# Kernel optimization log

Hardware: AMD Instinct MI355X
Metric: run time of the kernel (lower is better)

Reference implementation:

```python
import jax, jax.numpy as jnp
import numpy as np

N_TOKENS, MODEL_DIM, NUM_EXPERTS = 65536, 1024, 64
CAPACITY_FACTOR = 1.0


def setup_inputs() -> dict:
    key = jax.random.key(0)
    k1, k2 = jax.random.split(key)
    x = jax.random.normal(k1, (N_TOKENS, MODEL_DIM), dtype=jnp.float32)
    # gate projection weight, torch Linear stores [out_features, in_features]
    wg = jax.random.normal(k2, (NUM_EXPERTS, MODEL_DIM), dtype=jnp.float32) * (1.0 / np.sqrt(MODEL_DIM))
    return {"x": x, "wg": wg}


def reference(x, wg):
    N, E = x.shape[0], wg.shape[0]
    logits = x @ wg.T                              # [N, E]
    # training-branch capacity: capacity_factor * ceil(N / E)
    capacity = int(CAPACITY_FACTOR * ((N + E - 1) // E))
    indices1_s = jnp.argmax(logits, axis=1)        # [N] top-1 expert per token
    gates = jax.nn.softmax(logits, axis=1)         # [N, E]
    mask1 = jax.nn.one_hot(indices1_s, E, dtype=gates.dtype)  # [N, E]
    gates1_s = jnp.sum(gates * mask1, axis=1)      # [N] gate value of chosen expert
    # locations1_s[i] = number of earlier tokens routed to the same expert
    # (exclusive prefix count = inclusive cumsum - 1 at the selected column)
    locations1 = jnp.cumsum(mask1, axis=0) - 1.0   # [N, E]
    locations1_s = jnp.sum(locations1 * mask1, axis=1).astype(jnp.int32)
    # auxiliary load-balance loss (float32 branch of the original)
    me = jnp.sum(gates, axis=0)                    # [E]
    ce = jnp.sum(mask1, axis=0)                    # [E]
    l_aux = jnp.sum(me * ce) * (E / (N * N))
    return (l_aux, indices1_s.astype(jnp.int32), capacity, locations1_s, gates1_s, E)
```

## Files before the change

### kernel.cpp

```cpp
#include <hip/hip_runtime.h>

#define NT 65536
#define MD 1024
#define NE 64
#define BK 32

__global__ __launch_bounds__(256) void gate_kernel(
    const float* __restrict__ x, const float* __restrict__ wg,
    float* __restrict__ out, int* __restrict__ idx_ws,
    float* __restrict__ me, float* __restrict__ ce)
{
    __shared__ __align__(16) float smem[2 * BK * 68];
    float (*as)[68] = (float (*)[68])smem;
    float (*bs)[68] = (float (*)[68])(smem + BK * 68);

    const int tid = threadIdx.x;
    const int tx = tid & 15;
    const int ty = tid >> 4;
    const int t0 = blockIdx.x * 64;

    float acc[4][4];
#pragma unroll
    for (int i = 0; i < 4; ++i)
#pragma unroll
        for (int j = 0; j < 4; ++j) acc[i][j] = 0.f;

    for (int k0 = 0; k0 < MD; k0 += BK) {
#pragma unroll
        for (int l = 0; l < 2; ++l) {
            int flat = tid + l * 256;
            int r = flat >> 3;
            int q = flat & 7;
            float4 v = *(const float4*)(x + (size_t)(t0 + r) * MD + k0 + q * 4);
            as[q * 4 + 0][r] = v.x; as[q * 4 + 1][r] = v.y;
            as[q * 4 + 2][r] = v.z; as[q * 4 + 3][r] = v.w;
            float4 w = *(const float4*)(wg + (size_t)r * MD + k0 + q * 4);
            bs[q * 4 + 0][r] = w.x; bs[q * 4 + 1][r] = w.y;
            bs[q * 4 + 2][r] = w.z; bs[q * 4 + 3][r] = w.w;
        }
        __syncthreads();
#pragma unroll
        for (int k = 0; k < BK; ++k) {
            float4 a = *(const float4*)&as[k][ty * 4];
            float4 b = *(const float4*)&bs[k][tx * 4];
            float av[4] = {a.x, a.y, a.z, a.w};
            float bv[4] = {b.x, b.y, b.z, b.w};
#pragma unroll
            for (int i = 0; i < 4; ++i)
#pragma unroll
                for (int j = 0; j < 4; ++j) acc[i][j] += av[i] * bv[j];
        }
        __syncthreads();
    }

    float* lt  = smem;
    float* inv = smem + 4160;
    int*   hist = (int*)(smem + 4224);

#pragma unroll
    for (int i = 0; i < 4; ++i)
#pragma unroll
        for (int j = 0; j < 4; ++j)
            lt[(ty * 4 + i) * 65 + tx * 4 + j] = acc[i][j];
    if (tid < NE) hist[tid] = 0;
    __syncthreads();

    if (tid < 64) {
        const int t = tid;
        float m = -1e30f; int am = 0;
        for (int e = 0; e < NE; ++e) {
            float v = lt[t * 65 + e];
            if (v > m) { m = v; am = e; }
        }
        float s = 0.f;
        for (int e = 0; e < NE; ++e) {
            float ev = __expf(lt[t * 65 + e] - m);
            lt[t * 65 + e] = ev;
            s += ev;
        }
        float g = 1.0f / s;
        int gt = t0 + t;
        out[1 + gt] = (float)am;
        out[2 + 2 * NT + gt] = g;
        idx_ws[gt] = am;
        atomicAdd(&hist[am], 1);
        inv[t] = g;
    }
    __syncthreads();

    if (tid < NE) {
        const int e = tid;
        float s = 0.f;
        for (int t = 0; t < 64; ++t) s += lt[t * 65 + e] * inv[t];
        atomicAdd(&me[e], s);
        atomicAdd(&ce[e], (float)hist[e]);
    }
}

__global__ __launch_bounds__(256) void locations_kernel(
    const int* __restrict__ idx, float* __restrict__ out)
{
    const int e = blockIdx.x;
    const int tid = threadIdx.x;
    const int lane = tid & 63;
    const int wave = tid >> 6;
    __shared__ int wpre[4];
    float* out_loc = out + 2 + NT;
    const int4* idx4 = (const int4*)idx;

    int running = 0;
    for (int c = 0; c < NT / 4096; ++c) {
        int base4 = c * 1024 + tid * 4;
        int4 v0 = idx4[base4 + 0];
        int4 v1 = idx4[base4 + 1];
        int4 v2 = idx4[base4 + 2];
        int4 v3 = idx4[base4 + 3];
        int vals[16] = {v0.x, v0.y, v0.z, v0.w, v1.x, v1.y, v1.z, v1.w,
                        v2.x, v2.y, v2.z, v2.w, v3.x, v3.y, v3.z, v3.w};
        unsigned mask = 0;
#pragma unroll
        for (int j = 0; j < 16; ++j)
            if (vals[j] == e) mask |= (1u << j);
        int cnt = __popc(mask);

        int scan = cnt;
#pragma unroll
        for (int d = 1; d < 64; d <<= 1) {
            int o = __shfl_up(scan, d, 64);
            if (lane >= d) scan += o;
        }
        if (lane == 63) wpre[wave] = scan;
        __syncthreads();
        int wprefix = 0;
#pragma unroll
        for (int w = 0; w < 4; ++w)
            if (w < wave) wprefix += wpre[w];
        int tot = wpre[0] + wpre[1] + wpre[2] + wpre[3];

        int myexcl = running + wprefix + (scan - cnt);
        int r = 0;
#pragma unroll
        for (int j = 0; j < 16; ++j) {
            if (mask & (1u << j)) {
                out_loc[c * 4096 + tid * 16 + j] = (float)(myexcl + r);
                ++r;
            }
        }
        running += tot;
        __syncthreads();
    }
}

__global__ void finalize_kernel(const float* __restrict__ me,
                                const float* __restrict__ ce,
                                float* __restrict__ out)
{
    int tid = threadIdx.x;
    float v = me[tid] * ce[tid];
#pragma unroll
    for (int d = 32; d > 0; d >>= 1) v += __shfl_down(v, d, 64);
    if (tid == 0) {
        out[0] = v * (float)((double)NE / ((double)NT * (double)NT));
        out[1 + NT] = 1024.0f;
        out[2 + 3 * NT] = 64.0f;
    }
}

extern "C" void kernel_launch(void* const* d_in, const int* in_sizes, int n_in,
                              void* d_out, int out_size, void* d_ws, size_t ws_size,
                              hipStream_t stream)
{
    const float* x  = (const float*)d_in[0];
    const float* wg = (const float*)d_in[1];
    float* out = (float*)d_out;

    int*   idx_ws = (int*)d_ws;
    float* me = (float*)((char*)d_ws + (size_t)NT * sizeof(int));
    float* ce = me + NE;

    hipMemsetAsync(me, 0, 2 * NE * sizeof(float), stream);
    gate_kernel<<<NT / 64, 256, 0, stream>>>(x, wg, out, idx_ws, me, ce);
    locations_kernel<<<NE, 256, 0, stream>>>(idx_ws, out);
    finalize_kernel<<<1, 64, 0, stream>>>(me, ce, out);
}
```

Before: 445.2 us.

## Double-buffer gate GEMM tiles and replace per-expert location scan with block histograms

The gate GEMM now prefetches the next K-slice into registers and stages it into a second shared-memory buffer, so global loads overlap compute and one barrier per iteration is removed. The location computation no longer has 64 blocks each rescanning all token indices. Instead each gate block records per-expert counts and in-block ranks via wave ballots, a small scan kernel prefix-sums the per-block histograms, and an emit kernel writes the final positions. This adds shared memory and a ballot loop in the gate epilogue, plus an extra kernel launch.

```diff
diff --git a/kernel.cpp b/kernel.cpp
--- a/kernel.cpp
+++ b/kernel.cpp
@@ -4,45 +4,68 @@
 #define MD 1024
 #define NE 64
 #define BK 32
+#define NBLK (NT / 64)
 
 __global__ __launch_bounds__(256) void gate_kernel(
     const float* __restrict__ x, const float* __restrict__ wg,
-    float* __restrict__ out, int* __restrict__ idx_ws,
-    float* __restrict__ me, float* __restrict__ ce)
-{
-    __shared__ __align__(16) float smem[2 * BK * 68];
-    float (*as)[68] = (float (*)[68])smem;
-    float (*bs)[68] = (float (*)[68])(smem + BK * 68);
+    float* __restrict__ out, unsigned* __restrict__ packed_ws,
+    int* __restrict__ hist_ws, float* __restrict__ me)
+{
+    __shared__ __align__(16) float smem[4 * BK * 68];
+    float (*as)[BK][68] = (float (*)[BK][68])smem;
+    float (*bs)[BK][68] = (float (*)[BK][68])(smem + 2 * BK * 68);
 
     const int tid = threadIdx.x;
     const int tx = tid & 15;
     const int ty = tid >> 4;
     const int t0 = blockIdx.x * 64;
 
+    const int r0 = tid >> 3, q0 = tid & 7;
+    const int r1 = r0 + 32,  q1 = q0;
+    const float* xa0 = x  + (size_t)(t0 + r0) * MD + q0 * 4;
+    const float* xa1 = x  + (size_t)(t0 + r1) * MD + q1 * 4;
+    const float* wa0 = wg + (size_t)r0 * MD + q0 * 4;
+    const float* wa1 = wg + (size_t)r1 * MD + q1 * 4;
+
+    float4 va0 = *(const float4*)(xa0);
+    float4 va1 = *(const float4*)(xa1);
+    float4 vw0 = *(const float4*)(wa0);
+    float4 vw1 = *(const float4*)(wa1);
+
+#define STAGE(buf)                                                      \
+    do {                                                                \
+        as[buf][q0 * 4 + 0][r0] = va0.x; as[buf][q0 * 4 + 1][r0] = va0.y; \
+        as[buf][q0 * 4 + 2][r0] = va0.z; as[buf][q0 * 4 + 3][r0] = va0.w; \
+        as[buf][q1 * 4 + 0][r1] = va1.x; as[buf][q1 * 4 + 1][r1] = va1.y; \
+        as[buf][q1 * 4 + 2][r1] = va1.z; as[buf][q1 * 4 + 3][r1] = va1.w; \
+        bs[buf][q0 * 4 + 0][r0] = vw0.x; bs[buf][q0 * 4 + 1][r0] = vw0.y; \
+        bs[buf][q0 * 4 + 2][r0] = vw0.z; bs[buf][q0 * 4 + 3][r0] = vw0.w; \
+        bs[buf][q1 * 4 + 0][r1] = vw1.x; bs[buf][q1 * 4 + 1][r1] = vw1.y; \
+        bs[buf][q1 * 4 + 2][r1] = vw1.z; bs[buf][q1 * 4 + 3][r1] = vw1.w; \
+    } while (0)
+
+    STAGE(0);
+    __syncthreads();
+
     float acc[4][4];
 #pragma unroll
     for (int i = 0; i < 4; ++i)
 #pragma unroll
         for (int j = 0; j < 4; ++j) acc[i][j] = 0.f;
 
-    for (int k0 = 0; k0 < MD; k0 += BK) {
-#pragma unroll
-        for (int l = 0; l < 2; ++l) {
-            int flat = tid + l * 256;
-            int r = flat >> 3;
-            int q = flat & 7;
-            float4 v = *(const float4*)(x + (size_t)(t0 + r) * MD + k0 + q * 4);
-            as[q * 4 + 0][r] = v.x; as[q * 4 + 1][r] = v.y;
-            as[q * 4 + 2][r] = v.z; as[q * 4 + 3][r] = v.w;
-            float4 w = *(const float4*)(wg + (size_t)r * MD + k0 + q * 4);
-            bs[q * 4 + 0][r] = w.x; bs[q * 4 + 1][r] = w.y;
-            bs[q * 4 + 2][r] = w.z; bs[q * 4 + 3][r] = w.w;
-        }
-        __syncthreads();
+    for (int it = 0; it < MD / BK; ++it) {
+        const int cur = it & 1;
+        if (it < MD / BK - 1) {
+            const int kn = (it + 1) * BK;
+            va0 = *(const float4*)(xa0 + kn);
+            va1 = *(const float4*)(xa1 + kn);
+            vw0 = *(const float4*)(wa0 + kn);
+            vw1 = *(const float4*)(wa1 + kn);
+        }
 #pragma unroll
         for (int k = 0; k < BK; ++k) {
-            float4 a = *(const float4*)&as[k][ty * 4];
-            float4 b = *(const float4*)&bs[k][tx * 4];
+            float4 a = *(const float4*)&as[cur][k][ty * 4];
+            float4 b = *(const float4*)&bs[cur][k][tx * 4];
             float av[4] = {a.x, a.y, a.z, a.w};
             float bv[4] = {b.x, b.y, b.z, b.w};
 #pragma unroll
@@ -50,19 +73,21 @@
 #pragma unroll
                 for (int j = 0; j < 4; ++j) acc[i][j] += av[i] * bv[j];
         }
+        if (it < MD / BK - 1) {
+            const int nb = cur ^ 1;
+            STAGE(nb);
+        }
         __syncthreads();
     }
 
     float* lt  = smem;
     float* inv = smem + 4160;
-    int*   hist = (int*)(smem + 4224);
 
 #pragma unroll
     for (int i = 0; i < 4; ++i)
 #pragma unroll
         for (int j = 0; j < 4; ++j)
             lt[(ty * 4 + i) * 65 + tx * 4 + j] = acc[i][j];
-    if (tid < NE) hist[tid] = 0;
     __syncthreads();
 
     if (tid < 64) {
@@ -79,12 +104,20 @@
             s += ev;
         }
         float g = 1.0f / s;
-        int gt = t0 + t;
+        const int gt = t0 + t;
         out[1 + gt] = (float)am;
         out[2 + 2 * NT + gt] = g;
-        idx_ws[gt] = am;
-        atomicAdd(&hist[am], 1);
         inv[t] = g;
+
+        const unsigned long long below = (1ull << t) - 1ull;
+        int rank = 0, mycnt = 0;
+        for (int e = 0; e < NE; ++e) {
+            unsigned long long msk = __ballot(am == e);
+            if (t == e)  mycnt = (int)__popcll(msk);
+            if (am == e) rank  = (int)__popcll(msk & below);
+        }
+        packed_ws[gt] = (unsigned)am | ((unsigned)rank << 8);
+        hist_ws[blockIdx.x * NE + t] = mycnt;
     }
     __syncthreads();
 
@@ -93,62 +126,54 @@
         float s = 0.f;
         for (int t = 0; t < 64; ++t) s += lt[t * 65 + e] * inv[t];
         atomicAdd(&me[e], s);
-        atomicAdd(&ce[e], (float)hist[e]);
-    }
-}
-
-__global__ __launch_bounds__(256) void locations_kernel(
-    const int* __restrict__ idx, float* __restrict__ out)
+    }
+}
+
+__global__ __launch_bounds__(256) void scan_kernel(
+    int* __restrict__ hist_ws, float* __restrict__ ce)
 {
     const int e = blockIdx.x;
     const int tid = threadIdx.x;
-    const int lane = tid & 63;
-    const int wave = tid >> 6;
-    __shared__ int wpre[4];
-    float* out_loc = out + 2 + NT;
-    const int4* idx4 = (const int4*)idx;
-
-    int running = 0;
-    for (int c = 0; c < NT / 4096; ++c) {
-        int base4 = c * 1024 + tid * 4;
-        int4 v0 = idx4[base4 + 0];
-        int4 v1 = idx4[base4 + 1];
-        int4 v2 = idx4[base4 + 2];
-        int4 v3 = idx4[base4 + 3];
-        int vals[16] = {v0.x, v0.y, v0.z, v0.w, v1.x, v1.y, v1.z, v1.w,
-                        v2.x, v2.y, v2.z, v2.w, v3.x, v3.y, v3.z, v3.w};
-        unsigned mask = 0;
-#pragma unroll
-        for (int j = 0; j < 16; ++j)
-            if (vals[j] == e) mask |= (1u << j);
-        int cnt = __popc(mask);
-
-        int scan = cnt;
-#pragma unroll
-        for (int d = 1; d < 64; d <<= 1) {
-            int o = __shfl_up(scan, d, 64);
-            if (lane >= d) scan += o;
-        }
-        if (lane == 63) wpre[wave] = scan;
-        __syncthreads();
-        int wprefix = 0;
-#pragma unroll
-        for (int w = 0; w < 4; ++w)
-            if (w < wave) wprefix += wpre[w];
-        int tot = wpre[0] + wpre[1] + wpre[2] + wpre[3];
-
-        int myexcl = running + wprefix + (scan - cnt);
-        int r = 0;
-#pragma unroll
-        for (int j = 0; j < 16; ++j) {
-            if (mask & (1u << j)) {
-                out_loc[c * 4096 + tid * 16 + j] = (float)(myexcl + r);
-                ++r;
-            }
-        }
-        running += tot;
-        __syncthreads();
-    }
+    const int lane = tid & 63, wave = tid >> 6;
+    __shared__ int wtot[4];
+
+    int h[4];
+#pragma unroll
+    for (int j = 0; j < 4; ++j) h[j] = hist_ws[(tid * 4 + j) * NE + e];
+    int s = h[0] + h[1] + h[2] + h[3];
+
+    int scan = s;
+#pragma unroll
+    for (int d = 1; d < 64; d <<= 1) {
+        int o = __shfl_up(scan, d, 64);
+        if (lane >= d) scan += o;
+    }
+    if (lane == 63) wtot[wave] = scan;
+    __syncthreads();
+    int wpre = 0;
+#pragma unroll
+    for (int w = 0; w < 4; ++w)
+        if (w < wave) wpre += wtot[w];
+
+    int run = wpre + scan - s;
+#pragma unroll
+    for (int j = 0; j < 4; ++j) {
+        hist_ws[(tid * 4 + j) * NE + e] = run;
+        run += h[j];
+    }
+    if (tid == 255) ce[e] = (float)run;
+}
+
+__global__ __launch_bounds__(256) void emit_kernel(
+    const unsigned* __restrict__ packed_ws, const int* __restrict__ offs_ws,
+    float* __restrict__ out)
+{
+    const int i = blockIdx.x * 256 + threadIdx.x;
+    const unsigned p = packed_ws[i];
+    const int am = (int)(p & 63u);
+    const int rank = (int)(p >> 8);
+    const int b = i >> 6;
+    out[2 + NT + i] = (float)(offs_ws[b * NE + am] + rank);
 }
 
 __global__ void finalize_kernel(const float* __restrict__ me,
@@ -174,12 +199,14 @@
     const float* wg = (const float*)d_in[1];
     float* out = (float*)d_out;
 
-    int*   idx_ws = (int*)d_ws;
-    float* me = (float*)((char*)d_ws + (size_t)NT * sizeof(int));
+    unsigned* packed_ws = (unsigned*)d_ws;
+    int* hist_ws = (int*)((char*)d_ws + (size_t)NT * 4);
+    float* me = (float*)((char*)d_ws + (size_t)NT * 4 + (size_t)NBLK * NE * 4);
     float* ce = me + NE;
 
-    hipMemsetAsync(me, 0, 2 * NE * sizeof(float), stream);
-    gate_kernel<<<NT / 64, 256, 0, stream>>>(x, wg, out, idx_ws, me, ce);
-    locations_kernel<<<NE, 256, 0, stream>>>(idx_ws, out);
+    hipMemsetAsync(me, 0, NE * sizeof(float), stream);
+    gate_kernel<<<NBLK, 256, 0, stream>>>(x, wg, out, packed_ws, hist_ws, me);
+    scan_kernel<<<NE, 256, 0, stream>>>(hist_ws, ce);
+    emit_kernel<<<NT / 256, 256, 0, stream>>>(packed_ws, hist_ws, out);
     finalize_kernel<<<1, 64, 0, stream>>>(me, ce, out);
 }
```

Result: faster. 408.8 us (-8.2%).
